# Optimization experiments

Measured on AMD Instinct MI355X. Metric: run time of the kernel, lower is better.

## Reference

```python
import jax, jax.numpy as jnp
import numpy as np
import math

EPS = 1e-5
GROUPS = 32

def group_norm(x, gamma, beta, groups=GROUPS, eps=EPS):
    B, C, H, W = x.shape
    xr = x.reshape(B, groups, C // groups, H, W)
    m = xr.mean(axis=(2, 3, 4), keepdims=True)
    v = xr.var(axis=(2, 3, 4), keepdims=True)
    xr = (xr - m) * jax.lax.rsqrt(v + eps)
    x = xr.reshape(B, C, H, W)
    return x * gamma[None, :, None, None] + beta[None, :, None, None]

def swish(x):
    return x * jax.nn.sigmoid(x)

def conv2d(x, w, b=None, padding='SAME'):
    # x: NCHW, w: OIHW
    y = jax.lax.conv_general_dilated(x, w, window_strides=(1, 1), padding=padding,
                                     dimension_numbers=('NCHW', 'OIHW', 'NCHW'))
    if b is not None:
        y = y + b[None, :, None, None]
    return y

def setup_inputs() -> dict:
    key = jax.random.key(0)
    ks = jax.random.split(key, 24)
    B, C, H, W = 16, 256, 32, 32
    NE = 256  # noise_level_emb_dim
    s = 0.02
    inp = {
        'x': jax.random.normal(ks[0], (B, C, H, W), jnp.float32),
        'time_emb': jax.random.normal(ks[1], (B, NE), jnp.float32),
        'c': jax.random.normal(ks[2], (B, C, H, W), jnp.float32),
        # block1: GroupNorm + Swish + Conv3x3(dim -> dim_out)
        'gn1_g': jnp.ones((C,), jnp.float32),
        'gn1_b': jnp.zeros((C,), jnp.float32),
        'conv1_w': jax.random.normal(ks[3], (C, C, 3, 3), jnp.float32) * s,
        'conv1_b': jnp.zeros((C,), jnp.float32),
        # FeatureWiseAffine linear (use_affine_level=False): Linear(NE -> dim_out)
        'noise_w': jax.random.normal(ks[4], (C, NE), jnp.float32) * s,
        'noise_b': jnp.zeros((C,), jnp.float32),
        # block2: GroupNorm + Swish + Conv3x3(dim_out -> dim_out)
        'gn2_g': jnp.ones((C,), jnp.float32),
        'gn2_b': jnp.zeros((C,), jnp.float32),
        'conv2_w': jax.random.normal(ks[5], (C, C, 3, 3), jnp.float32) * s,
        'conv2_b': jnp.zeros((C,), jnp.float32),
        # c_func: Conv1x1(dim_out -> dim_out)
        'cfunc_w': jax.random.normal(ks[6], (C, C, 1, 1), jnp.float32) * s,
        'cfunc_b': jnp.zeros((C,), jnp.float32),
        # attention: GroupNorm, qkv Conv1x1 (no bias), out Conv1x1
        'attn_gn_g': jnp.ones((C,), jnp.float32),
        'attn_gn_b': jnp.zeros((C,), jnp.float32),
        'qkv_w': jax.random.normal(ks[7], (3 * C, C, 1, 1), jnp.float32) * s,
        'out_w': jax.random.normal(ks[8], (C, C, 1, 1), jnp.float32) * s,
        'out_b': jnp.zeros((C,), jnp.float32),
    }
    return inp

def reference(x, time_emb, c,
              gn1_g, gn1_b, conv1_w, conv1_b,
              noise_w, noise_b,
              gn2_g, gn2_b, conv2_w, conv2_b,
              cfunc_w, cfunc_b,
              attn_gn_g, attn_gn_b, qkv_w, out_w, out_b):
    B, C, H, W = x.shape
    # ---- ResnetBlock ----
    h = conv2d(swish(group_norm(x, gn1_g, gn1_b)), conv1_w, conv1_b)
    # FeatureWiseAffine (additive): h + Linear(time_emb) broadcast over HxW
    h = h + (time_emb @ noise_w.T + noise_b)[:, :, None, None]
    h = conv2d(swish(group_norm(h, gn2_g, gn2_b)), conv2_w, conv2_b)
    h = conv2d(c, cfunc_w, cfunc_b) + h
    h = h + x  # res_conv is Identity since dim == dim_out
    # ---- SelfAttention (n_head=1) ----
    n = group_norm(h, attn_gn_g, attn_gn_b)
    qkv = conv2d(n, qkv_w)                       # [B, 3C, H, W]
    q, k, v = jnp.split(qkv.reshape(B, 3 * C, H * W), 3, axis=1)  # each [B, C, HW]
    scores = jnp.einsum('bcs,bct->bst', q, k) / math.sqrt(C)      # [B, HW, HW]
    attn = jax.nn.softmax(scores, axis=-1)
    o = jnp.einsum('bst,bct->bcs', attn, v).reshape(B, C, H, W)
    o = conv2d(o, out_w, out_b)
    return o + h
```

## Files before the change

### kernel.cpp

```cpp
#include <hip/hip_runtime.h>
#include <hip/hip_bf16.h>
#include <math.h>

typedef __hip_bfloat16 bf16;
typedef short short8 __attribute__((ext_vector_type(8)));
typedef float floatx4 __attribute__((ext_vector_type(4)));

#define NB 16
#define NC 256
#define NHW 1024
#define NNE 256
#define NP (NB*NC*NHW)

__device__ __forceinline__ unsigned short f2bu(float f){
  bf16 h = (bf16)f; return *(unsigned short*)&h;
}

__device__ __forceinline__ void gload_lds16(const short* g, short* l){
  __builtin_amdgcn_global_load_lds(
      (const __attribute__((address_space(1))) void*)g,
      (__attribute__((address_space(3))) void*)l, 16, 0, 0);
}

__global__ __launch_bounds__(256)
void prep_mega_kernel(const float* __restrict__ w1, const float* __restrict__ w2,
                      short* __restrict__ wp1, short* __restrict__ wp2,
                      float* __restrict__ st,
                      const float* __restrict__ wq, const float* __restrict__ wc,
                      const float* __restrict__ wo,
                      short* __restrict__ wqp, short* __restrict__ wcp,
                      short* __restrict__ wop,
                      const float* __restrict__ c_in, short* __restrict__ cp,
                      const float* __restrict__ emb, const float* __restrict__ nw,
                      const float* __restrict__ nb, float* __restrict__ na,
                      const float* __restrict__ x, const float* __restrict__ gn1_g,
                      const float* __restrict__ gn1_b, short* __restrict__ xp){
  __shared__ float smem[8224];
  const int blk = blockIdx.x, tid = threadIdx.x;

  if (blk < 512){
    int co = blk & 255;
    const float* w = (blk < 256) ? w1 : w2;
    short* wp = (blk < 256) ? wp1 : wp2;
    if (blk == 0){
      for (int i=tid;i<4096;i+=256) st[i] = 0.f;
    }
    float* tmp = smem;
    for (int i=tid;i<2304;i+=256) tmp[i] = w[(size_t)co*2304 + i];
    __syncthreads();
    for (int j=tid;j<2304;j+=256){
      int tap = j>>8, ci = j&255;
      wp[(((size_t)tap*8 + (ci>>5))*NC + co)*32 + (ci&31)] = (short)f2bu(tmp[ci*9 + tap]);
    }
  } else if (blk < 1792){
    int bq = blk - 512;
    if (bq < 768){
      float v = wq[(size_t)bq*256 + tid];
      wqp[(((size_t)(tid>>5))*768 + bq)*32 + (tid&31)] = (short)f2bu(v);
    } else if (bq < 1024){
      int co = bq - 768;
      float v = wc[(size_t)co*256 + tid];
      wcp[(((size_t)(tid>>5))*256 + co)*32 + (tid&31)] = (short)f2bu(v);
    } else {
      int co = bq - 1024;
      float v = wo[(size_t)co*256 + tid];
      wop[(((size_t)(tid>>5))*256 + co)*32 + (tid&31)] = (short)f2bu(v);
    }
  } else if (blk < 2304){
    int j = blk - 1792;
    int pxc = j&3, cc = (j>>2)&7, b = j>>5;
    float* ld = smem;
    size_t gbase = ((size_t)b*NC + cc*32)*NHW + pxc*256;
    for (int r=0;r<32;r++) ld[r*257 + tid] = c_in[gbase + (size_t)r*NHW + tid];
    __syncthreads();
    short* dst = cp + (((size_t)b*8 + cc)*NHW + pxc*256)*32;
    for (int it=0;it<4;it++){
      int pxl = it*64 + (tid>>2), ckl = tid&3;
      short8 pk;
      #pragma unroll
      for (int e=0;e<8;e++) pk[e] = (short)f2bu(ld[(ckl*8+e)*257 + pxl]);
      *(short8*)(dst + (size_t)pxl*32 + ckl*8) = pk;
    }
  } else if (blk < 2320){
    int b = blk - 2304, c = tid;
    float* e = smem;
    e[c] = emb[b*NNE + c];
    __syncthreads();
    float acc = nb[c];
    for (int k=0;k<NNE;k++) acc += e[k]*nw[c*NNE+k];
    na[b*NC + c] = acc;
  } else {
    int j = blk - 2320;
    int b = j >> 5, g = j & 31;
    const int GSZ = 8*NHW;
    size_t base = ((size_t)b*NC + g*8)*NHW;
    float s = 0.f, ss = 0.f;
    for (int i = tid; i < GSZ; i += 256){
      float v = x[base+i];
      s += v; ss += v*v;
    }
    float* rs = smem; float* rq = smem + 256;
    rs[tid] = s; rq[tid] = ss;
    __syncthreads();
    for (int off=128; off>0; off>>=1){
      if (tid < off){ rs[tid]+=rs[tid+off]; rq[tid]+=rq[tid+off]; }
      __syncthreads();
    }
    float mean = rs[0] * (1.f/GSZ);
    float var  = rq[0] * (1.f/GSZ) - mean*mean;
    float inv  = rsqrtf(var + 1e-5f);
    float gm[8], bt[8];
    #pragma unroll
    for (int jj=0;jj<8;jj++){ gm[jj] = gn1_g[g*8+jj]*inv; bt[jj] = gn1_b[g*8+jj]; }
    short* dst = xp + (((size_t)b*8 + (g>>2))*NHW)*32 + (g&3)*8;
    for (int px = tid; px < NHW; px += 256){
      short8 pk;
      #pragma unroll
      for (int jj=0;jj<8;jj++){
        float v = (x[base + jj*NHW + px] - mean)*gm[jj] + bt[jj];
        v = v / (1.f + __expf(-v));
        pk[jj] = (short)f2bu(v);
      }
      *(short8*)(dst + (size_t)px*32) = pk;
    }
  }
}

template<bool SWISH>
__global__ void gn_post_kernel(const float* __restrict__ src, const float* __restrict__ st,
                               const float* __restrict__ gamma, const float* __restrict__ beta,
                               short* __restrict__ xp){
  int b = blockIdx.x >> 5, g = blockIdx.x & 31;
  size_t base = ((size_t)b*NC + g*8)*NHW;
  int tid = threadIdx.x;
  float s  = st[(b*32+g)*2+0];
  float ss = st[(b*32+g)*2+1];
  float mean = s * (1.f/8192.f);
  float var  = ss * (1.f/8192.f) - mean*mean;
  float inv  = rsqrtf(var + 1e-5f);
  float gm[8], bt[8];
  #pragma unroll
  for (int j=0;j<8;j++){ gm[j] = gamma[g*8+j]*inv; bt[j] = beta[g*8+j]; }
  short* dst = xp + (((size_t)b*8 + (g>>2))*NHW)*32 + (g&3)*8;
  for (int px = tid; px < NHW; px += 256){
    short8 pk;
    #pragma unroll
    for (int j=0;j<8;j++){
      float v = (src[base + j*NHW + px] - mean)*gm[j] + bt[j];
      if (SWISH) v = v / (1.f + __expf(-v));
      pk[j] = (short)f2bu(v);
    }
    *(short8*)(dst + (size_t)px*32) = pk;
  }
}

template<int NSTEP>
__global__ __launch_bounds__(256,3)
void conv3_mfma_kernel(const short* __restrict__ xp, const short* __restrict__ wp,
                       const float* __restrict__ bias, const float* __restrict__ bias_bc,
                       const float* __restrict__ addf, float* __restrict__ out,
                       float* __restrict__ st, const short* __restrict__ zpad,
                       const short* __restrict__ cp2, const short* __restrict__ wcp2,
                       const float* __restrict__ bias2){
  const int b = blockIdx.z, bx = blockIdx.x, by = blockIdx.y;
  const int tid = threadIdx.x, wave = tid>>6, lane = tid&63;
  const int quad = lane>>4, lm = lane&15;
  const int co0 = by*64;
  const int px0 = bx*128, yb = bx*4;

  __shared__ short Sb0[12288], Sb1[12288];

  const int rowt = tid>>3;
  const int g2   = (tid&7) ^ ((tid>>3)&7);
  const int kq2  = g2 & 3;
  const int ccs2 = g2 >> 2;
  const size_t b8 = (size_t)b*8*NHW*32;

  auto STAGE = [&](int j, short* S){
    if constexpr (NSTEP > 36){
      if (j >= 36){
        const int cc = j - 36;
        const short* wsrc = wcp2 + (size_t)(cc*2 + ccs2)*8192 + (co0 + rowt)*32 + kq2*8;
        #pragma unroll
        for (int i=0;i<2;i++)
          gload_lds16(wsrc + i*(32*32), S + tid*8 + i*2048);
        const short* xstep = cp2 + b8 + (size_t)(cc*2 + ccs2)*(NHW*32);
        #pragma unroll
        for (int i=0;i<4;i++)
          gload_lds16(xstep + ((yb+i)*32 + rowt)*32 + kq2*8, S + 4096 + tid*8 + i*2048);
        return;
      }
    }
    const int tap = j>>2, ccp = j&3;
    const int dyp = (tap*11)>>5;
    const int dx  = tap - dyp*3 - 1;
    const int dy  = dyp - 1;
    const short* wsrc = wp + (size_t)(tap*8 + ccp*2 + ccs2)*8192 + (co0 + rowt)*32 + kq2*8;
    #pragma unroll
    for (int i=0;i<2;i++)
      gload_lds16(wsrc + i*(32*32), S + tid*8 + i*2048);
    const short* xstep = xp + b8 + (size_t)(ccp*2 + ccs2)*(NHW*32);
    const int xx = rowt + dx;
    const bool xok = (unsigned)xx < 32u;
    #pragma unroll
    for (int i=0;i<4;i++){
      const int y = yb + i + dy;
      const short* src = (xok && (unsigned)y < 32u)
                       ? (xstep + (y*32 + xx)*32 + kq2*8)
                       : (zpad + kq2*8);
      gload_lds16(src, S + 4096 + tid*8 + i*2048);
    }
  };

  floatx4 acc[4][2];
  #pragma unroll
  for (int mt=0;mt<4;mt++)
    #pragma unroll
    for (int nt=0;nt<2;nt++) acc[mt][nt] = (floatx4){0.f,0.f,0.f,0.f};

  const int sl = lm & 7;
  auto STEP = [&](int j, short* S){
    asm volatile("s_waitcnt vmcnt(6)" ::: "memory");
    __builtin_amdgcn_s_barrier();
    __builtin_amdgcn_sched_barrier(0);
    short8 Af[2][4], Bf[2][2];
    #pragma unroll
    for (int ka=0;ka<2;ka++){
      const int slot = ((ka*4 + quad) ^ sl) << 3;
      #pragma unroll
      for (int mt=0;mt<4;mt++)
        Af[ka][mt] = *(const short8*)(S + (mt*16+lm)*64 + slot);
      #pragma unroll
      for (int nt=0;nt<2;nt++)
        Bf[ka][nt] = *(const short8*)(S + 4096 + (wave*32 + nt*16 + lm)*64 + slot);
    }
    asm volatile("s_waitcnt lgkmcnt(0)" ::: "memory");
    __builtin_amdgcn_sched_barrier(0);
    __builtin_amdgcn_s_barrier();
    int jn = j + 2; if (jn > NSTEP-1) jn = NSTEP-1;
    STAGE(jn, S);
    __builtin_amdgcn_s_setprio(1);
    #pragma unroll
    for (int ka=0;ka<2;ka++)
      #pragma unroll
      for (int mt=0;mt<4;mt++)
        #pragma unroll
        for (int nt=0;nt<2;nt++)
          acc[mt][nt] = __builtin_amdgcn_mfma_f32_16x16x32_bf16(Af[ka][mt], Bf[ka][nt], acc[mt][nt], 0,0,0);
    __builtin_amdgcn_s_setprio(0);
  };

  STAGE(0, Sb0); STAGE(1, Sb1);
  for (int jt=0; jt<36; jt+=2){
    STEP(jt+0, Sb0);
    STEP(jt+1, Sb1);
  }
  if constexpr (NSTEP == 40){
    STEP(36, Sb0);
    STEP(37, Sb1);
    STEP(38, Sb0);
    STEP(39, Sb1);
  }

  float gs[4], gq[4];
  #pragma unroll
  for (int mt=0;mt<4;mt++){ gs[mt]=0.f; gq[mt]=0.f; }
  #pragma unroll
  for (int mt=0;mt<4;mt++){
    #pragma unroll
    for (int r=0;r<4;r++){
      int co = co0 + mt*16 + quad*4 + r;
      float bb = bias[co] + (bias2 ? bias2[co] : 0.f) + (bias_bc ? bias_bc[b*NC + co] : 0.f);
      size_t ob = ((size_t)b*NC + co)*NHW + px0 + wave*32;
      #pragma unroll
      for (int nt=0;nt<2;nt++){
        size_t oi = ob + nt*16 + lm;
        float v = acc[mt][nt][r] + bb;
        if (addf) v += addf[oi];
        out[oi] = v;
        gs[mt] += v; gq[mt] += v*v;
      }
    }
  }
  #pragma unroll
  for (int mt=0;mt<4;mt++){
    float s = gs[mt], q = gq[mt];
    #pragma unroll
    for (int o=1;o<32;o<<=1){ s += __shfl_xor(s, o, 64); q += __shfl_xor(q, o, 64); }
    if ((lane&31) == 0){
      int g = (co0>>3) + mt*2 + (quad>>1);
      atomicAdd(&st[(b*32+g)*2+0], s);
      atomicAdd(&st[(b*32+g)*2+1], q);
    }
  }
}

__global__ __launch_bounds__(256)
void gemm_qkv_kernel(const short* __restrict__ ntp, const short* __restrict__ wqp,
                     short* __restrict__ qp, short* __restrict__ kp, short* __restrict__ vp){
  const int b = blockIdx.z;
  const int tid = threadIdx.x, wave = tid>>6, lane = tid&63;
  const int quad = lane>>4, lm = lane&15;
  const int M0 = blockIdx.y*128 + (wave>>1)*64;
  const int N0 = blockIdx.x*128 + (wave&1)*64;
  floatx4 acc[4][4];
  #pragma unroll
  for (int mt=0;mt<4;mt++)
    #pragma unroll
    for (int nt=0;nt<4;nt++) acc[mt][nt] = (floatx4){0.f,0.f,0.f,0.f};
  #pragma unroll
  for (int kk=0;kk<8;kk++){
    short8 af[4], bfr[4];
    #pragma unroll
    for (int mt=0;mt<4;mt++)
      af[mt] = *(const short8*)(wqp + ((size_t)kk*768 + M0 + mt*16 + lm)*32 + quad*8);
    #pragma unroll
    for (int nt=0;nt<4;nt++)
      bfr[nt] = *(const short8*)(ntp + (((size_t)b*8 + kk)*NHW + N0 + nt*16 + lm)*32 + quad*8);
    #pragma unroll
    for (int mt=0;mt<4;mt++)
      #pragma unroll
      for (int nt=0;nt<4;nt++)
        acc[mt][nt] = __builtin_amdgcn_mfma_f32_16x16x32_bf16(af[mt], bfr[nt], acc[mt][nt], 0,0,0);
  }
  #pragma unroll
  for (int mt=0;mt<4;mt++){
    int co_base = M0 + mt*16 + quad*4;
    int sec = co_base >> 8;
    int c = co_base & 255;
    #pragma unroll
    for (int nt=0;nt<4;nt++){
      int s = N0 + nt*16 + lm;
      if (sec < 2){
        unsigned short t0 = f2bu(acc[mt][nt][0]), t1 = f2bu(acc[mt][nt][1]);
        unsigned short t2 = f2bu(acc[mt][nt][2]), t3 = f2bu(acc[mt][nt][3]);
        uint2 w2; w2.x = ((unsigned)t1<<16)|t0; w2.y = ((unsigned)t3<<16)|t2;
        short* dst = (sec==0) ? qp : kp;
        *(uint2*)(dst + (((size_t)b*8 + (c>>5))*NHW + s)*32 + (c&31)) = w2;
      } else {
        #pragma unroll
        for (int r=0;r<4;r++)
          vp[(((size_t)b*32 + (s>>5))*NC + c + r)*32 + (s&31)] = (short)f2bu(acc[mt][nt][r]);
      }
    }
  }
}

__global__ __launch_bounds__(1024)
void attn_mfma_kernel(const short* __restrict__ qp, const short* __restrict__ kp,
                      const short* __restrict__ vp, short* __restrict__ op){
  const int bx = blockIdx.x;
  const int b = bx & 15;
  const int s0 = (bx >> 4) * 64;
  const int tid = threadIdx.x, wave = tid>>6, lane = tid&63;
  const int quad = lane>>4, lm = lane&15;

  __shared__ short P[64*1024];
  __shared__ float red[64][16];
  __shared__ float fred[64];

  floatx4 sc[4][4];
  #pragma unroll
  for (int rt=0;rt<4;rt++)
    #pragma unroll
    for (int ti=0;ti<4;ti++) sc[rt][ti] = (floatx4){0.f,0.f,0.f,0.f};

  const int colb = wave*64;
  #pragma unroll
  for (int h=0;h<8;h++){
    const size_t hb = ((size_t)b*8 + h)*NHW;
    short8 aq[4], kf[4];
    #pragma unroll
    for (int rt=0;rt<4;rt++)
      aq[rt] = *(const short8*)(qp + (hb + s0 + rt*16 + lm)*32 + quad*8);
    #pragma unroll
    for (int ti=0;ti<4;ti++)
      kf[ti] = *(const short8*)(kp + (hb + colb + ti*16 + lm)*32 + quad*8);
    #pragma unroll
    for (int rt=0;rt<4;rt++)
      #pragma unroll
      for (int ti=0;ti<4;ti++)
        sc[rt][ti] = __builtin_amdgcn_mfma_f32_16x16x32_bf16(aq[rt], kf[ti], sc[rt][ti], 0,0,0);
  }

  const float scale = 0.0625f;
  float mx[4][4];
  #pragma unroll
  for (int rt=0;rt<4;rt++)
    #pragma unroll
    for (int r=0;r<4;r++) mx[rt][r] = -1e30f;
  #pragma unroll
  for (int rt=0;rt<4;rt++)
    #pragma unroll
    for (int ti=0;ti<4;ti++)
      #pragma unroll
      for (int r=0;r<4;r++){
        float v = sc[rt][ti][r]*scale;
        sc[rt][ti][r] = v;
        mx[rt][r] = fmaxf(mx[rt][r], v);
      }
  #pragma unroll
  for (int o=1;o<16;o<<=1)
    #pragma unroll
    for (int rt=0;rt<4;rt++)
      #pragma unroll
      for (int r=0;r<4;r++) mx[rt][r] = fmaxf(mx[rt][r], __shfl_xor(mx[rt][r], o, 64));
  if (lm==0){
    #pragma unroll
    for (int rt=0;rt<4;rt++)
      #pragma unroll
      for (int r=0;r<4;r++) red[rt*16 + quad*4 + r][wave] = mx[rt][r];
  }
  __syncthreads();
  {
    float v = red[tid>>4][tid&15];
    #pragma unroll
    for (int o=1;o<16;o<<=1) v = fmaxf(v, __shfl_xor(v, o, 64));
    if ((tid&15)==0) fred[tid>>4] = v;
  }
  __syncthreads();
  float fmr[4][4], sm[4][4];
  #pragma unroll
  for (int rt=0;rt<4;rt++)
    #pragma unroll
    for (int r=0;r<4;r++){ fmr[rt][r] = fred[rt*16 + quad*4 + r]; sm[rt][r] = 0.f; }
  #pragma unroll
  for (int rt=0;rt<4;rt++)
    #pragma unroll
    for (int ti=0;ti<4;ti++)
      #pragma unroll
      for (int r=0;r<4;r++){
        float e = __expf(sc[rt][ti][r] - fmr[rt][r]);
        sc[rt][ti][r] = e;
        sm[rt][r] += e;
      }
  #pragma unroll
  for (int o=1;o<16;o<<=1)
    #pragma unroll
    for (int rt=0;rt<4;rt++)
      #pragma unroll
      for (int r=0;r<4;r++) sm[rt][r] += __shfl_xor(sm[rt][r], o, 64);
  __syncthreads();
  if (lm==0){
    #pragma unroll
    for (int rt=0;rt<4;rt++)
      #pragma unroll
      for (int r=0;r<4;r++) red[rt*16 + quad*4 + r][wave] = sm[rt][r];
  }
  __syncthreads();
  {
    float v = red[tid>>4][tid&15];
    #pragma unroll
    for (int o=1;o<16;o<<=1) v += __shfl_xor(v, o, 64);
    if ((tid&15)==0) fred[tid>>4] = 1.f/v;
  }
  __syncthreads();
  float fir[4][4];
  #pragma unroll
  for (int rt=0;rt<4;rt++)
    #pragma unroll
    for (int r=0;r<4;r++) fir[rt][r] = fred[rt*16 + quad*4 + r];
  #pragma unroll
  for (int rt=0;rt<4;rt++)
    #pragma unroll
    for (int ti=0;ti<4;ti++)
      #pragma unroll
      for (int r=0;r<4;r++){
        int row = rt*16 + quad*4 + r;
        int col = colb + ti*16 + lm;
        int off = row*1024 + ((((col>>3) ^ (row&7))&127)<<3) + (col&7);
        P[off] = (short)f2bu(sc[rt][ti][r]*fir[rt][r]);
      }
  __syncthreads();

  const int cg = wave>>1, sh = wave&1;
  const int ch0 = cg*32;
  floatx4 oacc[2][2];
  #pragma unroll
  for (int mt=0;mt<2;mt++)
    #pragma unroll
    for (int nt=0;nt<2;nt++) oacc[mt][nt] = (floatx4){0.f,0.f,0.f,0.f};

  #pragma unroll
  for (int kk=0;kk<32;kk++){
    short8 pf[2], vf[2];
    #pragma unroll
    for (int mt=0;mt<2;mt++){
      int row = sh*32 + mt*16 + lm;
      int off = row*1024 + ((((kk*4 + quad) ^ (row&7))&127)<<3);
      pf[mt] = *(const short8*)(&P[off]);
    }
    #pragma unroll
    for (int nt=0;nt<2;nt++)
      vf[nt] = *(const short8*)(vp + (((size_t)b*32 + kk)*NC + ch0 + nt*16 + lm)*32 + quad*8);
    #pragma unroll
    for (int mt=0;mt<2;mt++)
      #pragma unroll
      for (int nt=0;nt<2;nt++)
        oacc[mt][nt] = __builtin_amdgcn_mfma_f32_16x16x32_bf16(pf[mt], vf[nt], oacc[mt][nt], 0,0,0);
  }

  #pragma unroll
  for (int nt=0;nt<2;nt++){
    int c = ch0 + nt*16 + lm;
    int cc = c>>5, cl = c&31;
    #pragma unroll
    for (int mt=0;mt<2;mt++)
      #pragma unroll
      for (int r=0;r<4;r++){
        int s = s0 + sh*32 + mt*16 + quad*4 + r;
        op[(((size_t)b*8 + cc)*NHW + s)*32 + cl] = (short)f2bu(oacc[mt][nt][r]);
      }
  }
}

__global__ __launch_bounds__(256)
void outproj_mfma_kernel(const short* __restrict__ op, const short* __restrict__ wop,
                         const float* __restrict__ obias, const float* __restrict__ h,
                         float* __restrict__ out){
  const int b = blockIdx.z;
  const int tid = threadIdx.x, wave = tid>>6, lane = tid&63;
  const int quad = lane>>4, lm = lane&15;
  const int M0 = blockIdx.y*128 + (wave>>1)*64;
  const int N0 = blockIdx.x*128 + (wave&1)*64;
  floatx4 acc[4][4];
  #pragma unroll
  for (int mt=0;mt<4;mt++)
    #pragma unroll
    for (int nt=0;nt<4;nt++) acc[mt][nt] = (floatx4){0.f,0.f,0.f,0.f};
  #pragma unroll
  for (int kk=0;kk<8;kk++){
    short8 af[4], bfr[4];
    #pragma unroll
    for (int mt=0;mt<4;mt++)
      af[mt] = *(const short8*)(wop + ((size_t)kk*256 + M0 + mt*16 + lm)*32 + quad*8);
    #pragma unroll
    for (int nt=0;nt<4;nt++)
      bfr[nt] = *(const short8*)(op + (((size_t)b*8 + kk)*NHW + N0 + nt*16 + lm)*32 + quad*8);
    #pragma unroll
    for (int mt=0;mt<4;mt++)
      #pragma unroll
      for (int nt=0;nt<4;nt++)
        acc[mt][nt] = __builtin_amdgcn_mfma_f32_16x16x32_bf16(af[mt], bfr[nt], acc[mt][nt], 0,0,0);
  }
  #pragma unroll
  for (int mt=0;mt<4;mt++){
    #pragma unroll
    for (int r=0;r<4;r++){
      int co = M0 + mt*16 + quad*4 + r;
      float bb = obias[co];
      size_t ob = ((size_t)b*NC + co)*NHW + N0;
      #pragma unroll
      for (int nt=0;nt<4;nt++){
        size_t oi = ob + nt*16 + lm;
        out[oi] = acc[mt][nt][r] + bb + h[oi];
      }
    }
  }
}

extern "C" void kernel_launch(void* const* d_in, const int* in_sizes, int n_in,
                              void* d_out, int out_size, void* d_ws, size_t ws_size,
                              hipStream_t stream){
  const float* x        = (const float*)d_in[0];
  const float* time_emb = (const float*)d_in[1];
  const float* c_in     = (const float*)d_in[2];
  const float* gn1_g    = (const float*)d_in[3];
  const float* gn1_b    = (const float*)d_in[4];
  const float* conv1_w  = (const float*)d_in[5];
  const float* conv1_b  = (const float*)d_in[6];
  const float* noise_w  = (const float*)d_in[7];
  const float* noise_b  = (const float*)d_in[8];
  const float* gn2_g    = (const float*)d_in[9];
  const float* gn2_b    = (const float*)d_in[10];
  const float* conv2_w  = (const float*)d_in[11];
  const float* conv2_b  = (const float*)d_in[12];
  const float* cfunc_w  = (const float*)d_in[13];
  const float* cfunc_b  = (const float*)d_in[14];
  const float* agn_g    = (const float*)d_in[15];
  const float* agn_b    = (const float*)d_in[16];
  const float* qkv_w    = (const float*)d_in[17];
  const float* out_w    = (const float*)d_in[18];
  const float* out_b    = (const float*)d_in[19];
  float* outp = (float*)d_out;

  float* ws = (float*)d_ws;
  float* buf_h = ws;
  float* buf_t = buf_h + NP;
  short* xpb   = (short*)(buf_t + NP);
  short* qp    = xpb + NP;
  short* kp    = qp + NP;
  short* vp    = kp + NP;
  short* wp1   = vp + NP;
  short* wp2   = wp1 + 589824;
  short* wqp   = wp2 + 589824;
  short* wcp   = wqp + 196608;
  short* wop   = wcp + 65536;
  float* na    = (float*)(wop + 65536);
  float* st    = na + NB*NC;
  float* st2   = st;
  float* st3   = st + 1024;
  const short* zpadp = (const short*)(st + 2048);
  short* cp    = (short*)buf_t;
  short* op    = (short*)buf_t;

  prep_mega_kernel<<<2832, 256, 0, stream>>>(
      conv1_w, conv2_w, wp1, wp2, st,
      qkv_w, cfunc_w, out_w, wqp, wcp, wop,
      c_in, cp,
      time_emb, noise_w, noise_b, na,
      x, gn1_g, gn1_b, xpb);
  conv3_mfma_kernel<36><<<dim3(8, 4, NB), 256, 0, stream>>>(
      xpb, wp1, conv1_b, na, nullptr, buf_h, st2, zpadp, nullptr, nullptr, nullptr);
  gn_post_kernel<true><<<NB*32, 256, 0, stream>>>(buf_h, st2, gn2_g, gn2_b, xpb);
  conv3_mfma_kernel<40><<<dim3(8, 4, NB), 256, 0, stream>>>(
      xpb, wp2, conv2_b, nullptr, x, buf_h, st3, zpadp, cp, wcp, cfunc_b);
  gn_post_kernel<false><<<NB*32, 256, 0, stream>>>(buf_h, st3, agn_g, agn_b, xpb);
  gemm_qkv_kernel<<<dim3(8,6,NB), 256, 0, stream>>>(xpb, wqp, qp, kp, vp);
  attn_mfma_kernel<<<256, 1024, 0, stream>>>(qp, kp, vp, op);
  outproj_mfma_kernel<<<dim3(8,2,NB), 256, 0, stream>>>(op, wop, out_b, buf_h, outp);
}
```

Baseline: 317.6 us.

## Fuse output projection into attention kernel via LDS-staged attention output

The attention kernel now writes its bf16 output tile into shared memory (reusing the P buffer) instead of global memory. It then performs the 1x1 output projection, bias add and residual add itself, and the separate outproj kernel launch is removed. This drops the global round trip of the attention output and one launch. In exchange, each attention block re-reads the full projection weights, the per-block projection GEMM is small, and an extra barrier is added.

```diff
diff --git a/kernel.cpp b/kernel.cpp
--- a/kernel.cpp
+++ b/kernel.cpp
@@ -348,7 +348,9 @@
 
 __global__ __launch_bounds__(1024)
 void attn_mfma_kernel(const short* __restrict__ qp, const short* __restrict__ kp,
-                      const short* __restrict__ vp, short* __restrict__ op){
+                      const short* __restrict__ vp, const short* __restrict__ wopp,
+                      const float* __restrict__ obias, const float* __restrict__ h,
+                      float* __restrict__ out){
   const int bx = blockIdx.x;
   const int b = bx & 15;
   const int s0 = (bx >> 4) * 64;
@@ -367,8 +369,8 @@
 
   const int colb = wave*64;
   #pragma unroll
-  for (int h=0;h<8;h++){
-    const size_t hb = ((size_t)b*8 + h)*NHW;
+  for (int h8=0;h8<8;h8++){
+    const size_t hb = ((size_t)b*8 + h8)*NHW;
     short8 aq[4], kf[4];
     #pragma unroll
     for (int rt=0;rt<4;rt++)
@@ -500,61 +502,44 @@
         oacc[mt][nt] = __builtin_amdgcn_mfma_f32_16x16x32_bf16(pf[mt], vf[nt], oacc[mt][nt], 0,0,0);
   }
 
+  __syncthreads();
   #pragma unroll
   for (int nt=0;nt<2;nt++){
-    int c = ch0 + nt*16 + lm;
-    int cc = c>>5, cl = c&31;
+    int cl = nt*16 + lm;
     #pragma unroll
     for (int mt=0;mt<2;mt++)
       #pragma unroll
       for (int r=0;r<4;r++){
-        int s = s0 + sh*32 + mt*16 + quad*4 + r;
-        op[(((size_t)b*8 + cc)*NHW + s)*32 + cl] = (short)f2bu(oacc[mt][nt][r]);
-      }
-  }
-}
-
-__global__ __launch_bounds__(256)
-void outproj_mfma_kernel(const short* __restrict__ op, const short* __restrict__ wop,
-                         const float* __restrict__ obias, const float* __restrict__ h,
-                         float* __restrict__ out){
-  const int b = blockIdx.z;
-  const int tid = threadIdx.x, wave = tid>>6, lane = tid&63;
-  const int quad = lane>>4, lm = lane&15;
-  const int M0 = blockIdx.y*128 + (wave>>1)*64;
-  const int N0 = blockIdx.x*128 + (wave&1)*64;
-  floatx4 acc[4][4];
-  #pragma unroll
-  for (int mt=0;mt<4;mt++)
-    #pragma unroll
-    for (int nt=0;nt<4;nt++) acc[mt][nt] = (floatx4){0.f,0.f,0.f,0.f};
+        int sl2 = sh*32 + mt*16 + quad*4 + r;
+        P[(cg*64 + sl2)*40 + cl] = (short)f2bu(oacc[mt][nt][r]);
+      }
+  }
+  __syncthreads();
+
+  const int cog = wave>>2, sg = wave&3;
+  const int co0w = cog*64, sl0 = sg*16;
+  floatx4 pacc[4];
+  #pragma unroll
+  for (int mt=0;mt<4;mt++) pacc[mt] = (floatx4){0.f,0.f,0.f,0.f};
   #pragma unroll
   for (int kk=0;kk<8;kk++){
-    short8 af[4], bfr[4];
+    short8 af[4];
     #pragma unroll
     for (int mt=0;mt<4;mt++)
-      af[mt] = *(const short8*)(wop + ((size_t)kk*256 + M0 + mt*16 + lm)*32 + quad*8);
-    #pragma unroll
-    for (int nt=0;nt<4;nt++)
-      bfr[nt] = *(const short8*)(op + (((size_t)b*8 + kk)*NHW + N0 + nt*16 + lm)*32 + quad*8);
+      af[mt] = *(const short8*)(wopp + ((size_t)kk*256 + co0w + mt*16 + lm)*32 + quad*8);
+    short8 bfr = *(const short8*)(&P[(kk*64 + sl0 + lm)*40 + quad*8]);
     #pragma unroll
     for (int mt=0;mt<4;mt++)
-      #pragma unroll
-      for (int nt=0;nt<4;nt++)
-        acc[mt][nt] = __builtin_amdgcn_mfma_f32_16x16x32_bf16(af[mt], bfr[nt], acc[mt][nt], 0,0,0);
+      pacc[mt] = __builtin_amdgcn_mfma_f32_16x16x32_bf16(af[mt], bfr, pacc[mt], 0,0,0);
   }
   #pragma unroll
   for (int mt=0;mt<4;mt++){
     #pragma unroll
     for (int r=0;r<4;r++){
-      int co = M0 + mt*16 + quad*4 + r;
+      int co = co0w + mt*16 + quad*4 + r;
       float bb = obias[co];
-      size_t ob = ((size_t)b*NC + co)*NHW + N0;
-      #pragma unroll
-      for (int nt=0;nt<4;nt++){
-        size_t oi = ob + nt*16 + lm;
-        out[oi] = acc[mt][nt][r] + bb + h[oi];
-      }
+      size_t oi = ((size_t)b*NC + co)*NHW + s0 + sl0 + lm;
+      out[oi] = pacc[mt][r] + bb + h[oi];
     }
   }
 }
@@ -602,7 +587,6 @@
   float* st3   = st + 1024;
   const short* zpadp = (const short*)(st + 2048);
   short* cp    = (short*)buf_t;
-  short* op    = (short*)buf_t;
 
   prep_mega_kernel<<<2832, 256, 0, stream>>>(
       conv1_w, conv2_w, wp1, wp2, st,
@@ -617,6 +601,5 @@
       xpb, wp2, conv2_b, nullptr, x, buf_h, st3, zpadp, cp, wcp, cfunc_b);
   gn_post_kernel<false><<<NB*32, 256, 0, stream>>>(buf_h, st3, agn_g, agn_b, xpb);
   gemm_qkv_kernel<<<dim3(8,6,NB), 256, 0, stream>>>(xpb, wqp, qp, kp, vp);
-  attn_mfma_kernel<<<256, 1024, 0, stream>>>(qp, kp, vp, op);
-  outproj_mfma_kernel<<<dim3(8,2,NB), 256, 0, stream>>>(op, wop, out_b, buf_h, outp);
-}
+  attn_mfma_kernel<<<256, 1024, 0, stream>>>(qp, kp, vp, wop, out_b, buf_h, outp);
+}
```

Result: faster. 303.5 us (-4.4%).
